# Optimization experiments

Measured on AMD Instinct MI355X. Metric: run time of the kernel, lower is better.

## Reference

```python
import jax, jax.numpy as jnp
import numpy as np

D, H, F, L = 3, 3, 2048, 12  # d_model, nhead, dim_feedforward (torch default), num_layers
EPS = 1e-5


def _ln(x, w, b):
    m = x.mean(-1, keepdims=True)
    v = ((x - m) ** 2).mean(-1, keepdims=True)
    return (x - m) / jnp.sqrt(v + EPS) * w + b


def _mha(q_in, k_in, v_in, w, b, ow, ob):
    # w: [3D, D] packed qkv in_proj (torch layout), x: [T, B, D] seq-first
    qw, kw, vw = w[:D], w[D:2 * D], w[2 * D:]
    qb, kb, vb = b[:D], b[D:2 * D], b[2 * D:]
    q = q_in @ qw.T + qb
    k = k_in @ kw.T + kb
    v = v_in @ vw.T + vb
    hd = D // H  # head_dim = 1
    qh = q.reshape(q.shape[0], q.shape[1], H, hd)
    kh = k.reshape(k.shape[0], k.shape[1], H, hd)
    vh = v.reshape(v.shape[0], v.shape[1], H, hd)
    scores = jnp.einsum('qbhd,kbhd->bhqk', qh, kh) / np.sqrt(hd)
    attn = jax.nn.softmax(scores, axis=-1)
    o = jnp.einsum('bhqk,kbhd->qbhd', attn, vh).reshape(q_in.shape)
    return o @ ow.T + ob


def _encode(x, p):
    # post-norm TransformerEncoderLayer x12, then final encoder LayerNorm
    for i in range(L):
        x = _ln(x + _mha(x, x, x, p['sa_w'][i], p['sa_b'][i], p['sa_ow'][i], p['sa_ob'][i]),
                p['n1_w'][i], p['n1_b'][i])
        h = jax.nn.relu(x @ p['l1_w'][i].T + p['l1_b'][i]) @ p['l2_w'][i].T + p['l2_b'][i]
        x = _ln(x + h, p['n2_w'][i], p['n2_b'][i])
    return _ln(x, p['nf_w'], p['nf_b'])


def _decode(x, mem, p):
    # post-norm TransformerDecoderLayer x12 (no masks, matching the source), final LayerNorm
    for i in range(L):
        x = _ln(x + _mha(x, x, x, p['sa_w'][i], p['sa_b'][i], p['sa_ow'][i], p['sa_ob'][i]),
                p['n1_w'][i], p['n1_b'][i])
        x = _ln(x + _mha(x, mem, mem, p['ca_w'][i], p['ca_b'][i], p['ca_ow'][i], p['ca_ob'][i]),
                p['n2_w'][i], p['n2_b'][i])
        h = jax.nn.relu(x @ p['l1_w'][i].T + p['l1_b'][i]) @ p['l2_w'][i].T + p['l2_b'][i]
        x = _ln(x + h, p['n3_w'][i], p['n3_b'][i])
    return _ln(x, p['nf_w'], p['nf_b'])


def setup_inputs() -> dict:
    key = jax.random.key(0)
    ks = iter(jax.random.split(key, 64))

    def rn(shape, scale=0.1):
        return jax.random.normal(next(ks), shape, jnp.float32) * scale

    B, C, T = 16, 2, 32
    inp = {'src': rn((B, C, T), 1.0), 'angle': rn((B,), 1.0)}
    inp.update(dict(
        enc_sa_w=rn((L, 3 * D, D)), enc_sa_b=rn((L, 3 * D)), enc_sa_ow=rn((L, D, D)), enc_sa_ob=rn((L, D)),
        enc_l1_w=rn((L, F, D)), enc_l1_b=rn((L, F)), enc_l2_w=rn((L, D, F)), enc_l2_b=rn((L, D)),
        enc_n1_w=jnp.ones((L, D)), enc_n1_b=jnp.zeros((L, D)),
        enc_n2_w=jnp.ones((L, D)), enc_n2_b=jnp.zeros((L, D)),
        enc_nf_w=jnp.ones((D,)), enc_nf_b=jnp.zeros((D,)),
        dec_sa_w=rn((L, 3 * D, D)), dec_sa_b=rn((L, 3 * D)), dec_sa_ow=rn((L, D, D)), dec_sa_ob=rn((L, D)),
        dec_ca_w=rn((L, 3 * D, D)), dec_ca_b=rn((L, 3 * D)), dec_ca_ow=rn((L, D, D)), dec_ca_ob=rn((L, D)),
        dec_l1_w=rn((L, F, D)), dec_l1_b=rn((L, F)), dec_l2_w=rn((L, D, F)), dec_l2_b=rn((L, D)),
        dec_n1_w=jnp.ones((L, D)), dec_n1_b=jnp.zeros((L, D)),
        dec_n2_w=jnp.ones((L, D)), dec_n2_b=jnp.zeros((L, D)),
        dec_n3_w=jnp.ones((L, D)), dec_n3_b=jnp.zeros((L, D)),
        dec_nf_w=jnp.ones((D,)), dec_nf_b=jnp.zeros((D,)),
    ))
    return inp


def reference(src, angle,
              enc_sa_w, enc_sa_b, enc_sa_ow, enc_sa_ob, enc_l1_w, enc_l1_b, enc_l2_w, enc_l2_b,
              enc_n1_w, enc_n1_b, enc_n2_w, enc_n2_b, enc_nf_w, enc_nf_b,
              dec_sa_w, dec_sa_b, dec_sa_ow, dec_sa_ob, dec_ca_w, dec_ca_b, dec_ca_ow, dec_ca_ob,
              dec_l1_w, dec_l1_b, dec_l2_w, dec_l2_b,
              dec_n1_w, dec_n1_b, dec_n2_w, dec_n2_b, dec_n3_w, dec_n3_b, dec_nf_w, dec_nf_b):
    enc = dict(sa_w=enc_sa_w, sa_b=enc_sa_b, sa_ow=enc_sa_ow, sa_ob=enc_sa_ob,
               l1_w=enc_l1_w, l1_b=enc_l1_b, l2_w=enc_l2_w, l2_b=enc_l2_b,
               n1_w=enc_n1_w, n1_b=enc_n1_b, n2_w=enc_n2_w, n2_b=enc_n2_b,
               nf_w=enc_nf_w, nf_b=enc_nf_b)
    dec = dict(sa_w=dec_sa_w, sa_b=dec_sa_b, sa_ow=dec_sa_ow, sa_ob=dec_sa_ob,
               ca_w=dec_ca_w, ca_b=dec_ca_b, ca_ow=dec_ca_ow, ca_ob=dec_ca_ob,
               l1_w=dec_l1_w, l1_b=dec_l1_b, l2_w=dec_l2_w, l2_b=dec_l2_b,
               n1_w=dec_n1_w, n1_b=dec_n1_b, n2_w=dec_n2_w, n2_b=dec_n2_b,
               n3_w=dec_n3_w, n3_b=dec_n3_b, nf_w=dec_nf_w, nf_b=dec_nf_b)
    B, _, T = src.shape
    ang = jnp.broadcast_to(angle.reshape(B, 1, 1), (B, 1, T))
    s = jnp.concatenate([src, ang], axis=1)       # [B, 3, T]
    s = jnp.transpose(s, (2, 0, 1))                # [T, B, 3] seq-first
    mem = _encode(s, enc)                          # encoder depends only on src: compute once
    out0 = jnp.zeros_like(s).at[0].set(s[0])

    def step(out, t):
        pred = _decode(out, mem, dec)              # full no-mask decoder, as in the torch loop
        return out.at[t].set(pred[t]), None

    out, _ = jax.lax.scan(step, out0, jnp.arange(1, T))
    return jnp.transpose(out, (1, 2, 0))           # [B, 3, T]
```

## Files before the change

### kernel.cpp

```cpp
#include <hip/hip_runtime.h>
#include <math.h>

#define FF 2048
#define NL 12
#define NB 16
#define TT 32
#define EPS 1e-5f
#define LOG2E 1.44269504088896f

#if __has_builtin(__builtin_amdgcn_exp2f)
#define EXP2(x) __builtin_amdgcn_exp2f(x)
#else
#define EXP2(x) exp2f(x)
#endif

typedef float v2f __attribute__((ext_vector_type(2)));
__device__ __forceinline__ v2f mk2(float x){ v2f r; r.x = x; r.y = x; return r; }

__global__ __launch_bounds__(256) void prepack_kernel(
    const float* __restrict__ enc_l1_w, const float* __restrict__ enc_l1_b,
    const float* __restrict__ enc_l2_w,
    const float* __restrict__ dec_l1_w, const float* __restrict__ dec_l1_b,
    const float* __restrict__ dec_l2_w,
    float4* __restrict__ w_all)
{
    int idx = blockIdx.x * blockDim.x + threadIdx.x;
    if (idx >= 24 * 1024) return;
    int lay = idx >> 10;
    int fp  = idx & 1023;
    int f0  = 2*fp, f1 = 2*fp + 1;
    const float *w1, *b1, *w2;
    if (lay < NL) {
        w1 = enc_l1_w + (size_t)lay * FF * 3;
        b1 = enc_l1_b + (size_t)lay * FF;
        w2 = enc_l2_w + (size_t)lay * 3 * FF;
    } else {
        int l = lay - NL;
        w1 = dec_l1_w + (size_t)l * FF * 3;
        b1 = dec_l1_b + (size_t)l * FF;
        w2 = dec_l2_w + (size_t)l * 3 * FF;
    }
    float4* base = w_all + (size_t)lay * 4096;
    base[fp]        = make_float4(w1[f0*3+0], w1[f1*3+0], w1[f0*3+1], w1[f1*3+1]);
    base[1024 + fp] = make_float4(w1[f0*3+2], w1[f1*3+2], b1[f0],     b1[f1]);
    base[2048 + fp] = make_float4(w2[f0],     w2[f1],     w2[FF+f0],  w2[FF+f1]);
    base[3072 + fp] = make_float4(w2[2*FF+f0], w2[2*FF+f1], 0.f, 0.f);
}

struct __align__(16) SharedMem {
    float4 wbuf[2][4096];
    float4 x4[TT];
    float4 fred[TT][3];
    float4 outst[TT];
    float4 mem4[TT];
    float  kk[3][TT];
    float  vv[3][TT];
    float4 oo[TT];
    float4 oo2[TT];
    float  ck[NL][3][TT];
    float  cv[NL][3][TT];
};

__device__ __forceinline__ void ln3s(float y0, float y1, float y2,
    const float* __restrict__ w, const float* __restrict__ b,
    float& o0, float& o1, float& o2)
{
    float m  = (y0 + y1 + y2) * (1.0f / 3.0f);
    float d0 = y0 - m, d1 = y1 - m, d2 = y2 - m;
    float v  = (d0*d0 + d1*d1 + d2*d2) * (1.0f / 3.0f);
    float r  = __builtin_amdgcn_rsqf(v + EPS);
    o0 = d0 * r * w[0] + b[0];
    o1 = d1 * r * w[1] + b[1];
    o2 = d2 * r * w[2] + b[2];
}

template<int CTRL>
__device__ __forceinline__ float dpp_add(float v)
{
    int sh = __builtin_amdgcn_update_dpp(0, __float_as_int(v), CTRL, 0xF, 0xF, true);
    return v + __int_as_float(sh);
}

__device__ __forceinline__ float wave_sum64(float v)
{
    v = dpp_add<0x111>(v);
    v = dpp_add<0x112>(v);
    v = dpp_add<0x114>(v);
    v = dpp_add<0x118>(v);
    v = dpp_add<0x142>(v);
    v = dpp_add<0x143>(v);
    return v;
}

__device__ __forceinline__ float sum4(float4 r)
{
    return (r.x + r.y) + (r.z + r.w);
}

template<bool MASK>
__device__ __forceinline__ float attn_half(float qs,
    const float* __restrict__ k, const float* __restrict__ v,
    int half, int ntok, int rep, float repw)
{
    const float4* k4 = (const float4*)k;
    const float4* v4 = (const float4*)v;
    float den0 = 0.f, den1 = 0.f, nv0 = 0.f, nv1 = 0.f;
    #pragma unroll
    for (int jb = 0; jb < 4; ++jb) {
        float4 kq = k4[half*4 + jb];
        float4 vq = v4[half*4 + jb];
        const float kj[4] = {kq.x, kq.y, kq.z, kq.w};
        const float vj[4] = {vq.x, vq.y, vq.z, vq.w};
        #pragma unroll
        for (int u = 0; u < 4; ++u) {
            float w = EXP2(qs * kj[u]);
            if (MASK) {
                const int j = half*16 + jb*4 + u;
                w = (j < ntok) ? w : 0.f;
                w = (j == rep) ? w * repw : w;
            }
            if (jb & 1) { den1 += w; nv1 = fmaf(w, vj[u], nv1); }
            else        { den0 += w; nv0 = fmaf(w, vj[u], nv0); }
        }
    }
    float den = den0 + den1;
    float nv  = nv0 + nv1;
    den += __shfl_xor(den, 32, 64);
    nv  += __shfl_xor(nv , 32, 64);
    return nv * __builtin_amdgcn_rcpf(den);
}

template<int NII>
__device__ __forceinline__ void ffn_body(SharedMem& s, int tid,
    const float4* __restrict__ wb)
{
    const int flane = tid & 255;
    const int g     = tid >> 8;
    const int w4    = (tid >> 6) & 3;
    const int lane  = tid & 63;
    const v2f z2 = {0.f, 0.f};
    float X0[NII], X1[NII], X2[NII];
    v2f ac0[NII], ac1[NII], ac2[NII];
    #pragma unroll
    for (int ii = 0; ii < NII; ++ii) {
        float4 xt = s.x4[g + 4*ii];
        X0[ii] = xt.x; X1[ii] = xt.y; X2[ii] = xt.z;
        ac0[ii] = z2; ac1[ii] = z2; ac2[ii] = z2;
    }
    #pragma unroll
    for (int jp = 0; jp < 4; ++jp) {
        const int fp = flane + 256*jp;
        float4 A0 = wb[fp], A1 = wb[1024+fp];
        float4 C0 = wb[2048+fp], C1 = wb[3072+fp];
        v2f ax = {A0.x, A0.y}, ay = {A0.z, A0.w};
        v2f az = {A1.x, A1.y}, ab = {A1.z, A1.w};
        v2f cx = {C0.x, C0.y}, cy = {C0.z, C0.w};
        v2f cz = {C1.x, C1.y};
        #pragma unroll
        for (int ii = 0; ii < NII; ++ii) {
            v2f h2 = __builtin_elementwise_fma(ax, mk2(X0[ii]),
                     __builtin_elementwise_fma(ay, mk2(X1[ii]),
                     __builtin_elementwise_fma(az, mk2(X2[ii]), ab)));
            h2 = __builtin_elementwise_max(h2, z2);
            ac0[ii] = __builtin_elementwise_fma(cx, h2, ac0[ii]);
            ac1[ii] = __builtin_elementwise_fma(cy, h2, ac1[ii]);
            ac2[ii] = __builtin_elementwise_fma(cz, h2, ac2[ii]);
        }
    }
    #pragma unroll
    for (int ii = 0; ii < NII; ++ii) {
        const int t = g + 4*ii;
        float r0 = wave_sum64(ac0[ii].x + ac0[ii].y);
        float r1 = wave_sum64(ac1[ii].x + ac1[ii].y);
        float r2 = wave_sum64(ac2[ii].x + ac2[ii].y);
        if (lane == 63) {
            ((float*)&s.fred[t][0])[w4] = r0;
            ((float*)&s.fred[t][1])[w4] = r1;
            ((float*)&s.fred[t][2])[w4] = r2;
        }
    }
}

template<bool HAS_CA, bool MASK_SA>
__device__ __forceinline__ void run_layer(SharedMem& s, int tid,
    int ntok, int rep, float repw, int do_combine, int p,
    const float4* __restrict__ nw,
    const float* __restrict__ saw, const float* __restrict__ sab,
    const float* __restrict__ saow, const float* __restrict__ saob,
    const float* __restrict__ n1w, const float* __restrict__ n1b,
    const float* __restrict__ caw, const float* __restrict__ cab,
    const float* __restrict__ caow, const float* __restrict__ caob,
    const float* __restrict__ n2w, const float* __restrict__ n2b,
    const float* __restrict__ ckh, const float* __restrict__ cvh,
    const float* __restrict__ pl2b, const float* __restrict__ pnw,
    const float* __restrict__ pnb)
{
    const int wv   = tid >> 6;
    const int lane = tid & 63;
    const int q    = lane & 31;
    const int half = lane >> 5;
    float X0 = 0.f, X1 = 0.f, X2 = 0.f;
    float B0 = 0.f, B1 = 0.f, B2 = 0.f;

    if (wv >= 3) {
        for (int k = tid - 192; k < 2048; k += 832)
            s.wbuf[p ^ 1][k] = nw[k];
    } else {
        const int h = wv;
        float4 xa = s.x4[q];
        if (do_combine) {
            float f0 = sum4(s.fred[q][0]);
            float f1 = sum4(s.fred[q][1]);
            float f2 = sum4(s.fred[q][2]);
            ln3s(xa.x + f0 + pl2b[0], xa.y + f1 + pl2b[1],
                 xa.z + f2 + pl2b[2], pnw, pnb, X0, X1, X2);
        } else { X0 = xa.x; X1 = xa.y; X2 = xa.z; }
        if (lane < 32 && q < ntok) {
            s.kk[h][q] = sab[3+h] + saw[9+3*h]*X0  + saw[10+3*h]*X1 + saw[11+3*h]*X2;
            s.vv[h][q] = sab[6+h] + saw[18+3*h]*X0 + saw[19+3*h]*X1 + saw[20+3*h]*X2;
        }
        float qv = (sab[h] + saw[3*h]*X0 + saw[3*h+1]*X1 + saw[3*h+2]*X2) * LOG2E;
        float o = attn_half<MASK_SA>(qv, s.kk[h], s.vv[h], half, ntok, rep, repw);
        if (lane < 32 && q < ntok) ((float*)&s.oo[q])[h] = o;
    }
    __syncthreads();
    if (wv >= 3) {
        for (int k = 2048 + tid - 192; k < 4096; k += 832)
            s.wbuf[p ^ 1][k] = nw[k];
    } else {
        const int h = wv;
        float4 ov = s.oo[q];
        float y0 = X0 + saob[0] + saow[0]*ov.x + saow[1]*ov.y + saow[2]*ov.z;
        float y1 = X1 + saob[1] + saow[3]*ov.x + saow[4]*ov.y + saow[5]*ov.z;
        float y2 = X2 + saob[2] + saow[6]*ov.x + saow[7]*ov.y + saow[8]*ov.z;
        ln3s(y0, y1, y2, n1w, n1b, B0, B1, B2);
        if (!HAS_CA) {
            if (wv == 0 && lane < 32 && q < ntok)
                s.x4[q] = make_float4(B0, B1, B2, 0.f);
        } else {
            float cqv = (cab[h] + caw[3*h]*B0 + caw[3*h+1]*B1 + caw[3*h+2]*B2) * LOG2E;
            float oc = attn_half<false>(cqv, ckh + h*TT, cvh + h*TT, half, TT, -1, 1.f);
            if (lane < 32 && q < ntok) ((float*)&s.oo2[q])[h] = oc;
        }
    }
    __syncthreads();
    if (HAS_CA) {
        if (wv == 0 && lane < 32 && q < ntok) {
            float4 cv2 = s.oo2[q];
            float y0 = B0 + caob[0] + caow[0]*cv2.x + caow[1]*cv2.y + caow[2]*cv2.z;
            float y1 = B1 + caob[1] + caow[3]*cv2.x + caow[4]*cv2.y + caow[5]*cv2.z;
            float y2 = B2 + caob[2] + caow[6]*cv2.x + caow[7]*cv2.y + caow[8]*cv2.z;
            float a0, a1, a2;
            ln3s(y0, y1, y2, n2w, n2b, a0, a1, a2);
            s.x4[q] = make_float4(a0, a1, a2, 0.f);
        }
        __syncthreads();
    }
    const float4* wb = s.wbuf[p];
    if (ntok <= 8)       ffn_body<2>(s, tid, wb);
    else if (ntok <= 16) ffn_body<4>(s, tid, wb);
    else                 ffn_body<8>(s, tid, wb);
    __syncthreads();
}

__global__ __launch_bounds__(1024, 4) void seq_kernel(
    const float* __restrict__ src, const float* __restrict__ angle,
    const float* __restrict__ enc_sa_w, const float* __restrict__ enc_sa_b,
    const float* __restrict__ enc_sa_ow, const float* __restrict__ enc_sa_ob,
    const float* __restrict__ enc_l2_b,
    const float* __restrict__ enc_n1_w, const float* __restrict__ enc_n1_b,
    const float* __restrict__ enc_n2_w, const float* __restrict__ enc_n2_b,
    const float* __restrict__ enc_nf_w, const float* __restrict__ enc_nf_b,
    const float* __restrict__ dec_sa_w, const float* __restrict__ dec_sa_b,
    const float* __restrict__ dec_sa_ow, const float* __restrict__ dec_sa_ob,
    const float* __restrict__ dec_ca_w, const float* __restrict__ dec_ca_b,
    const float* __restrict__ dec_ca_ow, const float* __restrict__ dec_ca_ob,
    const float* __restrict__ dec_l2_b,
    const float* __restrict__ dec_n1_w, const float* __restrict__ dec_n1_b,
    const float* __restrict__ dec_n2_w, const float* __restrict__ dec_n2_b,
    const float* __restrict__ dec_n3_w, const float* __restrict__ dec_n3_b,
    const float* __restrict__ dec_nf_w, const float* __restrict__ dec_nf_b,
    const float4* __restrict__ w_all,
    float* __restrict__ out)
{
    __shared__ SharedMem s;
    const int tid = threadIdx.x;
    const int b   = blockIdx.x;

    for (int k = tid; k < 4096; k += 1024)
        s.wbuf[0][k] = w_all[k];
    if (tid < TT) {
        float x0 = src[b*64 + tid];
        float x1 = src[b*64 + 32 + tid];
        float x2 = angle[b];
        s.x4[tid] = make_float4(x0, x1, x2, 0.f);
        if (tid == 0) s.outst[0] = make_float4(x0, x1, x2, 0.f);
    }
    __syncthreads();

    int lp = 0;
    for (int i = 0; i < NL; ++i) {
        const float4* nw = w_all + (size_t)((i < 11) ? (i + 1) : 12) * 4096;
        const int pi = (i > 0) ? (i - 1) : 0;
        run_layer<false, false>(s, tid, TT, -1, 1.f, i > 0, lp & 1, nw,
            enc_sa_w + i*27, enc_sa_b + i*9, enc_sa_ow + i*9, enc_sa_ob + i*3,
            enc_n1_w + i*3, enc_n1_b + i*3,
            nullptr, nullptr, nullptr, nullptr, nullptr, nullptr,
            nullptr, nullptr,
            enc_l2_b + pi*3, enc_n2_w + pi*3, enc_n2_b + pi*3);
        ++lp;
    }
    if (tid < 32) {
        float4 xa = s.x4[tid];
        float f0 = sum4(s.fred[tid][0]);
        float f1 = sum4(s.fred[tid][1]);
        float f2 = sum4(s.fred[tid][2]);
        float o0, o1, o2, m0, m1, m2;
        ln3s(xa.x + f0 + enc_l2_b[33], xa.y + f1 + enc_l2_b[34],
             xa.z + f2 + enc_l2_b[35], enc_n2_w + 33, enc_n2_b + 33, o0, o1, o2);
        ln3s(o0, o1, o2, enc_nf_w, enc_nf_b, m0, m1, m2);
        s.mem4[tid] = make_float4(m0, m1, m2, 0.f);
        s.x4[tid]   = (tid == 0) ? s.outst[0] : make_float4(0.f, 0.f, 0.f, 0.f);
    }
    __syncthreads();

    for (int idx = tid; idx < NL * 96; idx += 1024) {
        const int lyr = idx / 96;
        const int r   = idx - lyr * 96;
        const int hh  = r >> 5;
        const int t   = r & 31;
        const float* w  = dec_ca_w + lyr*27;
        const float* bb = dec_ca_b + lyr*9;
        float4 mr = s.mem4[t];
        s.ck[lyr][hh][t] = bb[3+hh] + w[(3+hh)*3]*mr.x + w[(3+hh)*3+1]*mr.y + w[(3+hh)*3+2]*mr.z;
        s.cv[lyr][hh][t] = bb[6+hh] + w[(6+hh)*3]*mr.x + w[(6+hh)*3+1]*mr.y + w[(6+hh)*3+2]*mr.z;
    }
    __syncthreads();

    for (int t = 1; t < TT; ++t) {
        const int ntok = t + 1;
        for (int i = 0; i < NL; ++i) {
            const float4* nw = w_all + (size_t)(12 + ((i < 11) ? (i + 1) : 0)) * 4096;
            const int pi = (i > 0) ? (i - 1) : 0;
            run_layer<true, true>(s, tid, ntok, t, (float)(TT - t), i > 0, lp & 1, nw,
                dec_sa_w + i*27, dec_sa_b + i*9, dec_sa_ow + i*9, dec_sa_ob + i*3,
                dec_n1_w + i*3, dec_n1_b + i*3,
                dec_ca_w + i*27, dec_ca_b + i*9, dec_ca_ow + i*9, dec_ca_ob + i*3,
                dec_n2_w + i*3, dec_n2_b + i*3,
                &s.ck[i][0][0], &s.cv[i][0][0],
                dec_l2_b + pi*3, dec_n3_w + pi*3, dec_n3_b + pi*3);
            ++lp;
        }
        if (tid < 32) {
            if (tid == 0) {
                float4 xa = s.x4[t];
                float f0 = sum4(s.fred[t][0]);
                float f1 = sum4(s.fred[t][1]);
                float f2 = sum4(s.fred[t][2]);
                float o0, o1, o2, p0, p1, p2;
                ln3s(xa.x + f0 + dec_l2_b[33], xa.y + f1 + dec_l2_b[34],
                     xa.z + f2 + dec_l2_b[35], dec_n3_w + 33, dec_n3_b + 33,
                     o0, o1, o2);
                ln3s(o0, o1, o2, dec_nf_w, dec_nf_b, p0, p1, p2);
                s.outst[t] = make_float4(p0, p1, p2, 0.f);
            }
            s.x4[tid] = (tid <= t) ? s.outst[tid] : make_float4(0.f, 0.f, 0.f, 0.f);
        }
        __syncthreads();
    }

    if (tid < TT) {
        float4 o = s.outst[tid];
        out[b*96 +  0 + tid] = o.x;
        out[b*96 + 32 + tid] = o.y;
        out[b*96 + 64 + tid] = o.z;
    }
}

extern "C" void kernel_launch(void* const* d_in, const int* in_sizes, int n_in,
                              void* d_out, int out_size, void* d_ws, size_t ws_size,
                              hipStream_t stream) {
    const float* src      = (const float*)d_in[0];
    const float* angle    = (const float*)d_in[1];
    const float* enc_sa_w = (const float*)d_in[2];
    const float* enc_sa_b = (const float*)d_in[3];
    const float* enc_sa_ow= (const float*)d_in[4];
    const float* enc_sa_ob= (const float*)d_in[5];
    const float* enc_l1_w = (const float*)d_in[6];
    const float* enc_l1_b = (const float*)d_in[7];
    const float* enc_l2_w = (const float*)d_in[8];
    const float* enc_l2_b = (const float*)d_in[9];
    const float* enc_n1_w = (const float*)d_in[10];
    const float* enc_n1_b = (const float*)d_in[11];
    const float* enc_n2_w = (const float*)d_in[12];
    const float* enc_n2_b = (const float*)d_in[13];
    const float* enc_nf_w = (const float*)d_in[14];
    const float* enc_nf_b = (const float*)d_in[15];
    const float* dec_sa_w = (const float*)d_in[16];
    const float* dec_sa_b = (const float*)d_in[17];
    const float* dec_sa_ow= (const float*)d_in[18];
    const float* dec_sa_ob= (const float*)d_in[19];
    const float* dec_ca_w = (const float*)d_in[20];
    const float* dec_ca_b = (const float*)d_in[21];
    const float* dec_ca_ow= (const float*)d_in[22];
    const float* dec_ca_ob= (const float*)d_in[23];
    const float* dec_l1_w = (const float*)d_in[24];
    const float* dec_l1_b = (const float*)d_in[25];
    const float* dec_l2_w = (const float*)d_in[26];
    const float* dec_l2_b = (const float*)d_in[27];
    const float* dec_n1_w = (const float*)d_in[28];
    const float* dec_n1_b = (const float*)d_in[29];
    const float* dec_n2_w = (const float*)d_in[30];
    const float* dec_n2_b = (const float*)d_in[31];
    const float* dec_n3_w = (const float*)d_in[32];
    const float* dec_n3_b = (const float*)d_in[33];
    const float* dec_nf_w = (const float*)d_in[34];
    const float* dec_nf_b = (const float*)d_in[35];

    float4* w_all = (float4*)d_ws;

    prepack_kernel<<<(24 * 1024 + 255) / 256, 256, 0, stream>>>(
        enc_l1_w, enc_l1_b, enc_l2_w,
        dec_l1_w, dec_l1_b, dec_l2_w,
        w_all);

    seq_kernel<<<NB, 1024, 0, stream>>>(
        src, angle,
        enc_sa_w, enc_sa_b, enc_sa_ow, enc_sa_ob, enc_l2_b,
        enc_n1_w, enc_n1_b, enc_n2_w, enc_n2_b, enc_nf_w, enc_nf_b,
        dec_sa_w, dec_sa_b, dec_sa_ow, dec_sa_ob,
        dec_ca_w, dec_ca_b, dec_ca_ow, dec_ca_ob, dec_l2_b,
        dec_n1_w, dec_n1_b, dec_n2_w, dec_n2_b, dec_n3_w, dec_n3_b,
        dec_nf_w, dec_nf_b,
        (const float4*)w_all,
        (float*)d_out);
}
```

Measured before the change: 1.911 ms.

## Run all attention heads in one wave and keep decoder outputs in registers

Attention and layernorm work for all three heads and the cross-attention now run inside wave 0, with one barrier per layer instead of two or three. The other 15 waves prefetch the next layer's FFN weights during that time. The decoder output state moves from shared memory into per-lane registers and is updated lazily inside the first layer of the next step, which drops the per-step sync and copy. Masked key blocks beyond ntok are skipped and wave 0 gets raised priority. The trade-off is more serial work on a single wave per layer.

```diff
diff --git a/kernel.cpp b/kernel.cpp
--- a/kernel.cpp
+++ b/kernel.cpp
@@ -51,12 +51,9 @@
     float4 wbuf[2][4096];
     float4 x4[TT];
     float4 fred[TT][3];
-    float4 outst[TT];
     float4 mem4[TT];
     float  kk[3][TT];
     float  vv[3][TT];
-    float4 oo[TT];
-    float4 oo2[TT];
     float  ck[NL][3][TT];
     float  cv[NL][3][TT];
 };
@@ -107,20 +104,23 @@
     float den0 = 0.f, den1 = 0.f, nv0 = 0.f, nv1 = 0.f;
     #pragma unroll
     for (int jb = 0; jb < 4; ++jb) {
-        float4 kq = k4[half*4 + jb];
-        float4 vq = v4[half*4 + jb];
-        const float kj[4] = {kq.x, kq.y, kq.z, kq.w};
-        const float vj[4] = {vq.x, vq.y, vq.z, vq.w};
-        #pragma unroll
-        for (int u = 0; u < 4; ++u) {
-            float w = EXP2(qs * kj[u]);
-            if (MASK) {
-                const int j = half*16 + jb*4 + u;
-                w = (j < ntok) ? w : 0.f;
-                w = (j == rep) ? w * repw : w;
+        const int jbase = half*16 + jb*4;
+        if (!MASK || jbase < ntok) {
+            float4 kq = k4[half*4 + jb];
+            float4 vq = v4[half*4 + jb];
+            const float kj[4] = {kq.x, kq.y, kq.z, kq.w};
+            const float vj[4] = {vq.x, vq.y, vq.z, vq.w};
+            #pragma unroll
+            for (int u = 0; u < 4; ++u) {
+                float w = EXP2(qs * kj[u]);
+                if (MASK) {
+                    const int j = jbase + u;
+                    w = (j < ntok) ? w : 0.f;
+                    w = (j == rep) ? w * repw : w;
+                }
+                if (jb & 1) { den1 += w; nv1 = fmaf(w, vj[u], nv1); }
+                else        { den0 += w; nv0 = fmaf(w, vj[u], nv0); }
             }
-            if (jb & 1) { den1 += w; nv1 = fmaf(w, vj[u], nv1); }
-            else        { den0 += w; nv0 = fmaf(w, vj[u], nv0); }
         }
     }
     float den = den0 + den1;
@@ -181,9 +181,9 @@
     }
 }
 
-template<bool HAS_CA, bool MASK_SA>
+template<int MODE, bool HAS_CA, bool MASK_SA>
 __device__ __forceinline__ void run_layer(SharedMem& s, int tid,
-    int ntok, int rep, float repw, int do_combine, int p,
+    int ntok, int rep, float repw, int p,
     const float4* __restrict__ nw,
     const float* __restrict__ saw, const float* __restrict__ sab,
     const float* __restrict__ saow, const float* __restrict__ saob,
@@ -193,69 +193,80 @@
     const float* __restrict__ n2w, const float* __restrict__ n2b,
     const float* __restrict__ ckh, const float* __restrict__ cvh,
     const float* __restrict__ pl2b, const float* __restrict__ pnw,
-    const float* __restrict__ pnb)
+    const float* __restrict__ pnb,
+    const float* __restrict__ nfw, const float* __restrict__ nfb,
+    int tprev, int do_update,
+    float E0, float E1, float E2,
+    float& O0, float& O1, float& O2)
 {
     const int wv   = tid >> 6;
     const int lane = tid & 63;
     const int q    = lane & 31;
     const int half = lane >> 5;
-    float X0 = 0.f, X1 = 0.f, X2 = 0.f;
-    float B0 = 0.f, B1 = 0.f, B2 = 0.f;
-
-    if (wv >= 3) {
-        for (int k = tid - 192; k < 2048; k += 832)
+
+    if (wv >= 1) {
+        for (int k = tid - 64; k < 4096; k += 960)
             s.wbuf[p ^ 1][k] = nw[k];
     } else {
-        const int h = wv;
-        float4 xa = s.x4[q];
-        if (do_combine) {
+        __builtin_amdgcn_s_setprio(1);
+        float X0, X1, X2;
+        if (MODE == 0) {
+            X0 = E0; X1 = E1; X2 = E2;
+        } else if (MODE == 1) {
+            float4 xa = s.x4[q];
             float f0 = sum4(s.fred[q][0]);
             float f1 = sum4(s.fred[q][1]);
             float f2 = sum4(s.fred[q][2]);
             ln3s(xa.x + f0 + pl2b[0], xa.y + f1 + pl2b[1],
                  xa.z + f2 + pl2b[2], pnw, pnb, X0, X1, X2);
-        } else { X0 = xa.x; X1 = xa.y; X2 = xa.z; }
-        if (lane < 32 && q < ntok) {
-            s.kk[h][q] = sab[3+h] + saw[9+3*h]*X0  + saw[10+3*h]*X1 + saw[11+3*h]*X2;
-            s.vv[h][q] = sab[6+h] + saw[18+3*h]*X0 + saw[19+3*h]*X1 + saw[20+3*h]*X2;
-        }
-        float qv = (sab[h] + saw[3*h]*X0 + saw[3*h+1]*X1 + saw[3*h+2]*X2) * LOG2E;
-        float o = attn_half<MASK_SA>(qv, s.kk[h], s.vv[h], half, ntok, rep, repw);
-        if (lane < 32 && q < ntok) ((float*)&s.oo[q])[h] = o;
+        } else {
+            if (do_update && q == tprev) {
+                float4 xa = s.x4[q];
+                float f0 = sum4(s.fred[q][0]);
+                float f1 = sum4(s.fred[q][1]);
+                float f2 = sum4(s.fred[q][2]);
+                float o0, o1, o2;
+                ln3s(xa.x + f0 + pl2b[0], xa.y + f1 + pl2b[1],
+                     xa.z + f2 + pl2b[2], pnw, pnb, o0, o1, o2);
+                ln3s(o0, o1, o2, nfw, nfb, O0, O1, O2);
+            }
+            const bool rl = (q <= tprev);
+            X0 = rl ? O0 : 0.f; X1 = rl ? O1 : 0.f; X2 = rl ? O2 : 0.f;
+        }
+        if (half == 0 && q < ntok) {
+            for (int h = 0; h < 3; ++h) {
+                s.kk[h][q] = sab[3+h] + saw[9+3*h]*X0  + saw[10+3*h]*X1 + saw[11+3*h]*X2;
+                s.vv[h][q] = sab[6+h] + saw[18+3*h]*X0 + saw[19+3*h]*X1 + saw[20+3*h]*X2;
+            }
+        }
+        float oh[3];
+        for (int h = 0; h < 3; ++h) {
+            float qv = (sab[h] + saw[3*h]*X0 + saw[3*h+1]*X1 + saw[3*h+2]*X2) * LOG2E;
+            oh[h] = attn_half<MASK_SA>(qv, s.kk[h], s.vv[h], half, ntok, rep, repw);
+        }
+        float y0 = X0 + saob[0] + saow[0]*oh[0] + saow[1]*oh[1] + saow[2]*oh[2];
+        float y1 = X1 + saob[1] + saow[3]*oh[0] + saow[4]*oh[1] + saow[5]*oh[2];
+        float y2 = X2 + saob[2] + saow[6]*oh[0] + saow[7]*oh[1] + saow[8]*oh[2];
+        float B0, B1, B2;
+        ln3s(y0, y1, y2, n1w, n1b, B0, B1, B2);
+        if (HAS_CA) {
+            float oc[3];
+            for (int h = 0; h < 3; ++h) {
+                float cqv = (cab[h] + caw[3*h]*B0 + caw[3*h+1]*B1 + caw[3*h+2]*B2) * LOG2E;
+                oc[h] = attn_half<false>(cqv, ckh + h*TT, cvh + h*TT, half, TT, -1, 1.f);
+            }
+            float z0 = B0 + caob[0] + caow[0]*oc[0] + caow[1]*oc[1] + caow[2]*oc[2];
+            float z1 = B1 + caob[1] + caow[3]*oc[0] + caow[4]*oc[1] + caow[5]*oc[2];
+            float z2 = B2 + caob[2] + caow[6]*oc[0] + caow[7]*oc[1] + caow[8]*oc[2];
+            float A0, A1, A2;
+            ln3s(z0, z1, z2, n2w, n2b, A0, A1, A2);
+            if (half == 0 && q < ntok) s.x4[q] = make_float4(A0, A1, A2, 0.f);
+        } else {
+            if (half == 0 && q < ntok) s.x4[q] = make_float4(B0, B1, B2, 0.f);
+        }
+        __builtin_amdgcn_s_setprio(0);
     }
     __syncthreads();
-    if (wv >= 3) {
-        for (int k = 2048 + tid - 192; k < 4096; k += 832)
-            s.wbuf[p ^ 1][k] = nw[k];
-    } else {
-        const int h = wv;
-        float4 ov = s.oo[q];
-        float y0 = X0 + saob[0] + saow[0]*ov.x + saow[1]*ov.y + saow[2]*ov.z;
-        float y1 = X1 + saob[1] + saow[3]*ov.x + saow[4]*ov.y + saow[5]*ov.z;
-        float y2 = X2 + saob[2] + saow[6]*ov.x + saow[7]*ov.y + saow[8]*ov.z;
-        ln3s(y0, y1, y2, n1w, n1b, B0, B1, B2);
-        if (!HAS_CA) {
-            if (wv == 0 && lane < 32 && q < ntok)
-                s.x4[q] = make_float4(B0, B1, B2, 0.f);
-        } else {
-            float cqv = (cab[h] + caw[3*h]*B0 + caw[3*h+1]*B1 + caw[3*h+2]*B2) * LOG2E;
-            float oc = attn_half<false>(cqv, ckh + h*TT, cvh + h*TT, half, TT, -1, 1.f);
-            if (lane < 32 && q < ntok) ((float*)&s.oo2[q])[h] = oc;
-        }
-    }
-    __syncthreads();
-    if (HAS_CA) {
-        if (wv == 0 && lane < 32 && q < ntok) {
-            float4 cv2 = s.oo2[q];
-            float y0 = B0 + caob[0] + caow[0]*cv2.x + caow[1]*cv2.y + caow[2]*cv2.z;
-            float y1 = B1 + caob[1] + caow[3]*cv2.x + caow[4]*cv2.y + caow[5]*cv2.z;
-            float y2 = B2 + caob[2] + caow[6]*cv2.x + caow[7]*cv2.y + caow[8]*cv2.z;
-            float a0, a1, a2;
-            ln3s(y0, y1, y2, n2w, n2b, a0, a1, a2);
-            s.x4[q] = make_float4(a0, a1, a2, 0.f);
-        }
-        __syncthreads();
-    }
     const float4* wb = s.wbuf[p];
     if (ntok <= 8)       ffn_body<2>(s, tid, wb);
     else if (ntok <= 16) ffn_body<4>(s, tid, wb);
@@ -289,38 +300,54 @@
 
     for (int k = tid; k < 4096; k += 1024)
         s.wbuf[0][k] = w_all[k];
-    if (tid < TT) {
-        float x0 = src[b*64 + tid];
-        float x1 = src[b*64 + 32 + tid];
-        float x2 = angle[b];
-        s.x4[tid] = make_float4(x0, x1, x2, 0.f);
-        if (tid == 0) s.outst[0] = make_float4(x0, x1, x2, 0.f);
-    }
-    __syncthreads();
+
+    float E0 = 0.f, E1 = 0.f, E2 = 0.f, O0 = 0.f, O1 = 0.f, O2 = 0.f;
+    if (tid < 64) {
+        const int q = tid & 31;
+        E0 = src[b*64 + q];
+        E1 = src[b*64 + 32 + q];
+        E2 = angle[b];
+    }
 
     int lp = 0;
-    for (int i = 0; i < NL; ++i) {
+    {
+        const float4* nw0 = w_all + (size_t)1 * 4096;
+        run_layer<0, false, false>(s, tid, TT, -1, 1.f, 0, nw0,
+            enc_sa_w, enc_sa_b, enc_sa_ow, enc_sa_ob,
+            enc_n1_w, enc_n1_b,
+            nullptr, nullptr, nullptr, nullptr, nullptr, nullptr,
+            nullptr, nullptr,
+            nullptr, nullptr, nullptr, nullptr, nullptr,
+            -1, 0, E0, E1, E2, O0, O1, O2);
+        ++lp;
+    }
+    for (int i = 1; i < NL; ++i) {
         const float4* nw = w_all + (size_t)((i < 11) ? (i + 1) : 12) * 4096;
-        const int pi = (i > 0) ? (i - 1) : 0;
-        run_layer<false, false>(s, tid, TT, -1, 1.f, i > 0, lp & 1, nw,
+        run_layer<1, false, false>(s, tid, TT, -1, 1.f, lp & 1, nw,
             enc_sa_w + i*27, enc_sa_b + i*9, enc_sa_ow + i*9, enc_sa_ob + i*3,
             enc_n1_w + i*3, enc_n1_b + i*3,
             nullptr, nullptr, nullptr, nullptr, nullptr, nullptr,
             nullptr, nullptr,
-            enc_l2_b + pi*3, enc_n2_w + pi*3, enc_n2_b + pi*3);
+            enc_l2_b + (i-1)*3, enc_n2_w + (i-1)*3, enc_n2_b + (i-1)*3,
+            nullptr, nullptr,
+            -1, 0, 0.f, 0.f, 0.f, O0, O1, O2);
         ++lp;
     }
-    if (tid < 32) {
-        float4 xa = s.x4[tid];
-        float f0 = sum4(s.fred[tid][0]);
-        float f1 = sum4(s.fred[tid][1]);
-        float f2 = sum4(s.fred[tid][2]);
+
+    if (tid < 64) {
+        const int q = tid & 31;
+        float4 xa = s.x4[q];
+        float f0 = sum4(s.fred[q][0]);
+        float f1 = sum4(s.fred[q][1]);
+        float f2 = sum4(s.fred[q][2]);
         float o0, o1, o2, m0, m1, m2;
         ln3s(xa.x + f0 + enc_l2_b[33], xa.y + f1 + enc_l2_b[34],
              xa.z + f2 + enc_l2_b[35], enc_n2_w + 33, enc_n2_b + 33, o0, o1, o2);
         ln3s(o0, o1, o2, enc_nf_w, enc_nf_b, m0, m1, m2);
-        s.mem4[tid] = make_float4(m0, m1, m2, 0.f);
-        s.x4[tid]   = (tid == 0) ? s.outst[0] : make_float4(0.f, 0.f, 0.f, 0.f);
+        if (tid < 32) s.mem4[q] = make_float4(m0, m1, m2, 0.f);
+        O0 = (q == 0) ? E0 : 0.f;
+        O1 = (q == 0) ? E1 : 0.f;
+        O2 = (q == 0) ? E2 : 0.f;
     }
     __syncthreads();
 
@@ -339,41 +366,53 @@
 
     for (int t = 1; t < TT; ++t) {
         const int ntok = t + 1;
-        for (int i = 0; i < NL; ++i) {
+        const float rw = (float)(TT - t);
+        {
+            const float4* nw = w_all + (size_t)13 * 4096;
+            run_layer<2, true, true>(s, tid, ntok, t, rw, lp & 1, nw,
+                dec_sa_w, dec_sa_b, dec_sa_ow, dec_sa_ob,
+                dec_n1_w, dec_n1_b,
+                dec_ca_w, dec_ca_b, dec_ca_ow, dec_ca_ob,
+                dec_n2_w, dec_n2_b,
+                &s.ck[0][0][0], &s.cv[0][0][0],
+                dec_l2_b + 33, dec_n3_w + 33, dec_n3_b + 33,
+                dec_nf_w, dec_nf_b,
+                t - 1, (t >= 2) ? 1 : 0, 0.f, 0.f, 0.f, O0, O1, O2);
+            ++lp;
+        }
+        for (int i = 1; i < NL; ++i) {
             const float4* nw = w_all + (size_t)(12 + ((i < 11) ? (i + 1) : 0)) * 4096;
-            const int pi = (i > 0) ? (i - 1) : 0;
-            run_layer<true, true>(s, tid, ntok, t, (float)(TT - t), i > 0, lp & 1, nw,
+            run_layer<1, true, true>(s, tid, ntok, t, rw, lp & 1, nw,
                 dec_sa_w + i*27, dec_sa_b + i*9, dec_sa_ow + i*9, dec_sa_ob + i*3,
                 dec_n1_w + i*3, dec_n1_b + i*3,
                 dec_ca_w + i*27, dec_ca_b + i*9, dec_ca_ow + i*9, dec_ca_ob + i*3,
                 dec_n2_w + i*3, dec_n2_b + i*3,
                 &s.ck[i][0][0], &s.cv[i][0][0],
-                dec_l2_b + pi*3, dec_n3_w + pi*3, dec_n3_b + pi*3);
+                dec_l2_b + (i-1)*3, dec_n3_w + (i-1)*3, dec_n3_b + (i-1)*3,
+                nullptr, nullptr,
+                -1, 0, 0.f, 0.f, 0.f, O0, O1, O2);
             ++lp;
         }
+    }
+
+    if (tid < 64) {
+        const int q = tid & 31;
+        if (q == 31) {
+            float4 xa = s.x4[31];
+            float f0 = sum4(s.fred[31][0]);
+            float f1 = sum4(s.fred[31][1]);
+            float f2 = sum4(s.fred[31][2]);
+            float o0, o1, o2;
+            ln3s(xa.x + f0 + dec_l2_b[33], xa.y + f1 + dec_l2_b[34],
+                 xa.z + f2 + dec_l2_b[35], dec_n3_w + 33, dec_n3_b + 33,
+                 o0, o1, o2);
+            ln3s(o0, o1, o2, dec_nf_w, dec_nf_b, O0, O1, O2);
+        }
         if (tid < 32) {
-            if (tid == 0) {
-                float4 xa = s.x4[t];
-                float f0 = sum4(s.fred[t][0]);
-                float f1 = sum4(s.fred[t][1]);
-                float f2 = sum4(s.fred[t][2]);
-                float o0, o1, o2, p0, p1, p2;
-                ln3s(xa.x + f0 + dec_l2_b[33], xa.y + f1 + dec_l2_b[34],
-                     xa.z + f2 + dec_l2_b[35], dec_n3_w + 33, dec_n3_b + 33,
-                     o0, o1, o2);
-                ln3s(o0, o1, o2, dec_nf_w, dec_nf_b, p0, p1, p2);
-                s.outst[t] = make_float4(p0, p1, p2, 0.f);
-            }
-            s.x4[tid] = (tid <= t) ? s.outst[tid] : make_float4(0.f, 0.f, 0.f, 0.f);
-        }
-        __syncthreads();
-    }
-
-    if (tid < TT) {
-        float4 o = s.outst[tid];
-        out[b*96 +  0 + tid] = o.x;
-        out[b*96 + 32 + tid] = o.y;
-        out[b*96 + 64 + tid] = o.z;
+            out[b*96 +  0 + q] = O0;
+            out[b*96 + 32 + q] = O1;
+            out[b*96 + 64 + q] = O2;
+        }
     }
 }
 
```

After: 2.711 ms. 41.9% more time.

## Process two batch elements per block sharing FFN weight buffers

Applied to the files above, without the earlier changes.

Each 1024-thread block now handles two batch elements, so the grid shrinks from 16 to 8 blocks. Waves 0-2 and 3-5 run attention for element 0 and element 1, and the remaining waves prefetch the next layer's FFN weights. The FFN splits threads into two halves, one per element, each streaming all 2048 hidden units from the same shared weight buffer. The goal is to halve global weight traffic and barrier count per element, at the cost of half as many threads working on each element. Attention also skips key blocks past ntok.

```diff
diff --git a/kernel.cpp b/kernel.cpp
--- a/kernel.cpp
+++ b/kernel.cpp
@@ -49,16 +49,16 @@
 
 struct __align__(16) SharedMem {
     float4 wbuf[2][4096];
-    float4 x4[TT];
-    float4 fred[TT][3];
-    float4 outst[TT];
-    float4 mem4[TT];
-    float  kk[3][TT];
-    float  vv[3][TT];
-    float4 oo[TT];
-    float4 oo2[TT];
-    float  ck[NL][3][TT];
-    float  cv[NL][3][TT];
+    float4 x4[2][TT];
+    float  fred[2][TT][3][2];
+    float4 outst[2][TT];
+    float4 mem4[2][TT];
+    float  kk[2][3][TT];
+    float  vv[2][3][TT];
+    float4 oo[2][TT];
+    float4 oo2[2][TT];
+    float  ck[2][NL][3][TT];
+    float  cv[2][NL][3][TT];
 };
 
 __device__ __forceinline__ void ln3s(float y0, float y1, float y2,
@@ -92,10 +92,7 @@
     return v;
 }
 
-__device__ __forceinline__ float sum4(float4 r)
-{
-    return (r.x + r.y) + (r.z + r.w);
-}
+__device__ __forceinline__ float fr2(const float* p) { return p[0] + p[1]; }
 
 template<bool MASK>
 __device__ __forceinline__ float attn_half(float qs,
@@ -107,20 +104,23 @@
     float den0 = 0.f, den1 = 0.f, nv0 = 0.f, nv1 = 0.f;
     #pragma unroll
     for (int jb = 0; jb < 4; ++jb) {
-        float4 kq = k4[half*4 + jb];
-        float4 vq = v4[half*4 + jb];
-        const float kj[4] = {kq.x, kq.y, kq.z, kq.w};
-        const float vj[4] = {vq.x, vq.y, vq.z, vq.w};
-        #pragma unroll
-        for (int u = 0; u < 4; ++u) {
-            float w = EXP2(qs * kj[u]);
-            if (MASK) {
-                const int j = half*16 + jb*4 + u;
-                w = (j < ntok) ? w : 0.f;
-                w = (j == rep) ? w * repw : w;
+        const int jbase = half*16 + jb*4;
+        if (!MASK || jbase < ntok) {
+            float4 kq = k4[half*4 + jb];
+            float4 vq = v4[half*4 + jb];
+            const float kj[4] = {kq.x, kq.y, kq.z, kq.w};
+            const float vj[4] = {vq.x, vq.y, vq.z, vq.w};
+            #pragma unroll
+            for (int u = 0; u < 4; ++u) {
+                float w = EXP2(qs * kj[u]);
+                if (MASK) {
+                    const int j = jbase + u;
+                    w = (j < ntok) ? w : 0.f;
+                    w = (j == rep) ? w * repw : w;
+                }
+                if (jb & 1) { den1 += w; nv1 = fmaf(w, vj[u], nv1); }
+                else        { den0 += w; nv0 = fmaf(w, vj[u], nv0); }
             }
-            if (jb & 1) { den1 += w; nv1 = fmaf(w, vj[u], nv1); }
-            else        { den0 += w; nv0 = fmaf(w, vj[u], nv0); }
         }
     }
     float den = den0 + den1;
@@ -131,25 +131,26 @@
 }
 
 template<int NII>
-__device__ __forceinline__ void ffn_body(SharedMem& s, int tid,
+__device__ __forceinline__ void ffn_body2(SharedMem& s, int tid,
     const float4* __restrict__ wb)
 {
-    const int flane = tid & 255;
-    const int g     = tid >> 8;
-    const int w4    = (tid >> 6) & 3;
+    const int flane = tid & 127;
+    const int gi    = (tid >> 7) & 3;
+    const int e     = tid >> 9;
+    const int w2i   = (tid >> 6) & 1;
     const int lane  = tid & 63;
     const v2f z2 = {0.f, 0.f};
     float X0[NII], X1[NII], X2[NII];
     v2f ac0[NII], ac1[NII], ac2[NII];
     #pragma unroll
     for (int ii = 0; ii < NII; ++ii) {
-        float4 xt = s.x4[g + 4*ii];
+        float4 xt = s.x4[e][gi + 4*ii];
         X0[ii] = xt.x; X1[ii] = xt.y; X2[ii] = xt.z;
         ac0[ii] = z2; ac1[ii] = z2; ac2[ii] = z2;
     }
-    #pragma unroll
-    for (int jp = 0; jp < 4; ++jp) {
-        const int fp = flane + 256*jp;
+    #pragma unroll 2
+    for (int jp = 0; jp < 8; ++jp) {
+        const int fp = flane + 128*jp;
         float4 A0 = wb[fp], A1 = wb[1024+fp];
         float4 C0 = wb[2048+fp], C1 = wb[3072+fp];
         v2f ax = {A0.x, A0.y}, ay = {A0.z, A0.w};
@@ -169,21 +170,21 @@
     }
     #pragma unroll
     for (int ii = 0; ii < NII; ++ii) {
-        const int t = g + 4*ii;
+        const int t = gi + 4*ii;
         float r0 = wave_sum64(ac0[ii].x + ac0[ii].y);
         float r1 = wave_sum64(ac1[ii].x + ac1[ii].y);
         float r2 = wave_sum64(ac2[ii].x + ac2[ii].y);
         if (lane == 63) {
-            ((float*)&s.fred[t][0])[w4] = r0;
-            ((float*)&s.fred[t][1])[w4] = r1;
-            ((float*)&s.fred[t][2])[w4] = r2;
+            s.fred[e][t][0][w2i] = r0;
+            s.fred[e][t][1][w2i] = r1;
+            s.fred[e][t][2][w2i] = r2;
         }
     }
 }
 
 template<bool HAS_CA, bool MASK_SA>
 __device__ __forceinline__ void run_layer(SharedMem& s, int tid,
-    int ntok, int rep, float repw, int do_combine, int p,
+    int ntok, int rep, float repw, int do_combine, int p, int li,
     const float4* __restrict__ nw,
     const float* __restrict__ saw, const float* __restrict__ sab,
     const float* __restrict__ saow, const float* __restrict__ saob,
@@ -191,7 +192,6 @@
     const float* __restrict__ caw, const float* __restrict__ cab,
     const float* __restrict__ caow, const float* __restrict__ caob,
     const float* __restrict__ n2w, const float* __restrict__ n2b,
-    const float* __restrict__ ckh, const float* __restrict__ cvh,
     const float* __restrict__ pl2b, const float* __restrict__ pnw,
     const float* __restrict__ pnb)
 {
@@ -199,67 +199,69 @@
     const int lane = tid & 63;
     const int q    = lane & 31;
     const int half = lane >> 5;
+    const int e    = (wv >= 3) ? 1 : 0;
+    const int h    = wv - 3*e;
     float X0 = 0.f, X1 = 0.f, X2 = 0.f;
     float B0 = 0.f, B1 = 0.f, B2 = 0.f;
 
-    if (wv >= 3) {
-        for (int k = tid - 192; k < 2048; k += 832)
+    if (wv >= 6) {
+        for (int k = tid - 384; k < 2048; k += 640)
             s.wbuf[p ^ 1][k] = nw[k];
     } else {
-        const int h = wv;
-        float4 xa = s.x4[q];
+        float4 xa = s.x4[e][q];
         if (do_combine) {
-            float f0 = sum4(s.fred[q][0]);
-            float f1 = sum4(s.fred[q][1]);
-            float f2 = sum4(s.fred[q][2]);
+            float f0 = fr2(s.fred[e][q][0]);
+            float f1 = fr2(s.fred[e][q][1]);
+            float f2 = fr2(s.fred[e][q][2]);
             ln3s(xa.x + f0 + pl2b[0], xa.y + f1 + pl2b[1],
                  xa.z + f2 + pl2b[2], pnw, pnb, X0, X1, X2);
         } else { X0 = xa.x; X1 = xa.y; X2 = xa.z; }
         if (lane < 32 && q < ntok) {
-            s.kk[h][q] = sab[3+h] + saw[9+3*h]*X0  + saw[10+3*h]*X1 + saw[11+3*h]*X2;
-            s.vv[h][q] = sab[6+h] + saw[18+3*h]*X0 + saw[19+3*h]*X1 + saw[20+3*h]*X2;
+            s.kk[e][h][q] = sab[3+h] + saw[9+3*h]*X0  + saw[10+3*h]*X1 + saw[11+3*h]*X2;
+            s.vv[e][h][q] = sab[6+h] + saw[18+3*h]*X0 + saw[19+3*h]*X1 + saw[20+3*h]*X2;
         }
         float qv = (sab[h] + saw[3*h]*X0 + saw[3*h+1]*X1 + saw[3*h+2]*X2) * LOG2E;
-        float o = attn_half<MASK_SA>(qv, s.kk[h], s.vv[h], half, ntok, rep, repw);
-        if (lane < 32 && q < ntok) ((float*)&s.oo[q])[h] = o;
-    }
-    __syncthreads();
-    if (wv >= 3) {
-        for (int k = 2048 + tid - 192; k < 4096; k += 832)
+        float o = attn_half<MASK_SA>(qv, &s.kk[e][h][0], &s.vv[e][h][0],
+                                     half, ntok, rep, repw);
+        if (lane < 32 && q < ntok) ((float*)&s.oo[e][q])[h] = o;
+    }
+    __syncthreads();
+    if (wv >= 6) {
+        for (int k = 2048 + tid - 384; k < 4096; k += 640)
             s.wbuf[p ^ 1][k] = nw[k];
     } else {
-        const int h = wv;
-        float4 ov = s.oo[q];
+        float4 ov = s.oo[e][q];
         float y0 = X0 + saob[0] + saow[0]*ov.x + saow[1]*ov.y + saow[2]*ov.z;
         float y1 = X1 + saob[1] + saow[3]*ov.x + saow[4]*ov.y + saow[5]*ov.z;
         float y2 = X2 + saob[2] + saow[6]*ov.x + saow[7]*ov.y + saow[8]*ov.z;
         ln3s(y0, y1, y2, n1w, n1b, B0, B1, B2);
         if (!HAS_CA) {
-            if (wv == 0 && lane < 32 && q < ntok)
-                s.x4[q] = make_float4(B0, B1, B2, 0.f);
+            if (h == 0 && lane < 32 && q < ntok)
+                s.x4[e][q] = make_float4(B0, B1, B2, 0.f);
         } else {
             float cqv = (cab[h] + caw[3*h]*B0 + caw[3*h+1]*B1 + caw[3*h+2]*B2) * LOG2E;
-            float oc = attn_half<false>(cqv, ckh + h*TT, cvh + h*TT, half, TT, -1, 1.f);
-            if (lane < 32 && q < ntok) ((float*)&s.oo2[q])[h] = oc;
+            float oc = attn_half<false>(cqv, &s.ck[e][li][h][0], &s.cv[e][li][h][0],
+                                        half, TT, -1, 1.f);
+            if (lane < 32 && q < ntok) ((float*)&s.oo2[e][q])[h] = oc;
         }
     }
     __syncthreads();
     if (HAS_CA) {
-        if (wv == 0 && lane < 32 && q < ntok) {
-            float4 cv2 = s.oo2[q];
+        if (wv < 6 && h == 0 && lane < 32 && q < ntok) {
+            float4 cv2 = s.oo2[e][q];
             float y0 = B0 + caob[0] + caow[0]*cv2.x + caow[1]*cv2.y + caow[2]*cv2.z;
             float y1 = B1 + caob[1] + caow[3]*cv2.x + caow[4]*cv2.y + caow[5]*cv2.z;
             float y2 = B2 + caob[2] + caow[6]*cv2.x + caow[7]*cv2.y + caow[8]*cv2.z;
             float a0, a1, a2;
             ln3s(y0, y1, y2, n2w, n2b, a0, a1, a2);
-            s.x4[q] = make_float4(a0, a1, a2, 0.f);
+            s.x4[e][q] = make_float4(a0, a1, a2, 0.f);
         }
         __syncthreads();
     }
     const float4* wb = s.wbuf[p];
-    if (ntok <= 8)       ffn_body<2>(s, tid, wb);
-    else if (ntok <= 16) ffn_body<4>(s, tid, wb);
-    else                 ffn_body<8>(s, tid, wb);
+    if (ntok <= 8)       ffn_body2<2>(s, tid, wb);
+    else if (ntok <= 16) ffn_body2<4>(s, tid, wb);
+    else                 ffn_body2<8>(s, tid, wb);
     __syncthreads();
 }
 
@@ -285,16 +287,18 @@
 {
     __shared__ SharedMem s;
     const int tid = threadIdx.x;
-    const int b   = blockIdx.x;
+    const int b0  = blockIdx.x * 2;
 
     for (int k = tid; k < 4096; k += 1024)
         s.wbuf[0][k] = w_all[k];
-    if (tid < TT) {
-        float x0 = src[b*64 + tid];
-        float x1 = src[b*64 + 32 + tid];
-        float x2 = angle[b];
-        s.x4[tid] = make_float4(x0, x1, x2, 0.f);
-        if (tid == 0) s.outst[0] = make_float4(x0, x1, x2, 0.f);
+    if (tid < 64) {
+        const int e = tid >> 5;
+        const int q = tid & 31;
+        float x0 = src[(b0 + e)*64 + q];
+        float x1 = src[(b0 + e)*64 + 32 + q];
+        float x2 = angle[b0 + e];
+        s.x4[e][q] = make_float4(x0, x1, x2, 0.f);
+        if (q == 0) s.outst[e][0] = make_float4(x0, x1, x2, 0.f);
     }
     __syncthreads();
 
@@ -302,38 +306,42 @@
     for (int i = 0; i < NL; ++i) {
         const float4* nw = w_all + (size_t)((i < 11) ? (i + 1) : 12) * 4096;
         const int pi = (i > 0) ? (i - 1) : 0;
-        run_layer<false, false>(s, tid, TT, -1, 1.f, i > 0, lp & 1, nw,
+        run_layer<false, false>(s, tid, TT, -1, 1.f, i > 0, lp & 1, 0, nw,
             enc_sa_w + i*27, enc_sa_b + i*9, enc_sa_ow + i*9, enc_sa_ob + i*3,
             enc_n1_w + i*3, enc_n1_b + i*3,
             nullptr, nullptr, nullptr, nullptr, nullptr, nullptr,
-            nullptr, nullptr,
             enc_l2_b + pi*3, enc_n2_w + pi*3, enc_n2_b + pi*3);
         ++lp;
     }
-    if (tid < 32) {
-        float4 xa = s.x4[tid];
-        float f0 = sum4(s.fred[tid][0]);
-        float f1 = sum4(s.fred[tid][1]);
-        float f2 = sum4(s.fred[tid][2]);
+    if (tid < 256 && (tid >> 6) % 3 == 0 && (tid & 63) < 32) {
+        const int wv = tid >> 6;
+        const int e  = wv / 3;
+        const int q  = tid & 31;
+        float4 xa = s.x4[e][q];
+        float f0 = fr2(s.fred[e][q][0]);
+        float f1 = fr2(s.fred[e][q][1]);
+        float f2 = fr2(s.fred[e][q][2]);
         float o0, o1, o2, m0, m1, m2;
         ln3s(xa.x + f0 + enc_l2_b[33], xa.y + f1 + enc_l2_b[34],
              xa.z + f2 + enc_l2_b[35], enc_n2_w + 33, enc_n2_b + 33, o0, o1, o2);
         ln3s(o0, o1, o2, enc_nf_w, enc_nf_b, m0, m1, m2);
-        s.mem4[tid] = make_float4(m0, m1, m2, 0.f);
-        s.x4[tid]   = (tid == 0) ? s.outst[0] : make_float4(0.f, 0.f, 0.f, 0.f);
-    }
-    __syncthreads();
-
-    for (int idx = tid; idx < NL * 96; idx += 1024) {
-        const int lyr = idx / 96;
-        const int r   = idx - lyr * 96;
+        s.mem4[e][q] = make_float4(m0, m1, m2, 0.f);
+        s.x4[e][q]   = (q == 0) ? s.outst[e][0] : make_float4(0.f, 0.f, 0.f, 0.f);
+    }
+    __syncthreads();
+
+    for (int idx = tid; idx < 2 * NL * 96; idx += 1024) {
+        const int e   = idx / (NL * 96);
+        const int r0  = idx - e * NL * 96;
+        const int lyr = r0 / 96;
+        const int r   = r0 - lyr * 96;
         const int hh  = r >> 5;
         const int t   = r & 31;
         const float* w  = dec_ca_w + lyr*27;
         const float* bb = dec_ca_b + lyr*9;
-        float4 mr = s.mem4[t];
-        s.ck[lyr][hh][t] = bb[3+hh] + w[(3+hh)*3]*mr.x + w[(3+hh)*3+1]*mr.y + w[(3+hh)*3+2]*mr.z;
-        s.cv[lyr][hh][t] = bb[6+hh] + w[(6+hh)*3]*mr.x + w[(6+hh)*3+1]*mr.y + w[(6+hh)*3+2]*mr.z;
+        float4 mr = s.mem4[e][t];
+        s.ck[e][lyr][hh][t] = bb[3+hh] + w[(3+hh)*3]*mr.x + w[(3+hh)*3+1]*mr.y + w[(3+hh)*3+2]*mr.z;
+        s.cv[e][lyr][hh][t] = bb[6+hh] + w[(6+hh)*3]*mr.x + w[(6+hh)*3+1]*mr.y + w[(6+hh)*3+2]*mr.z;
     }
     __syncthreads();
 
@@ -342,38 +350,45 @@
         for (int i = 0; i < NL; ++i) {
             const float4* nw = w_all + (size_t)(12 + ((i < 11) ? (i + 1) : 0)) * 4096;
             const int pi = (i > 0) ? (i - 1) : 0;
-            run_layer<true, true>(s, tid, ntok, t, (float)(TT - t), i > 0, lp & 1, nw,
+            run_layer<true, true>(s, tid, ntok, t, (float)(TT - t), i > 0, lp & 1, i, nw,
                 dec_sa_w + i*27, dec_sa_b + i*9, dec_sa_ow + i*9, dec_sa_ob + i*3,
                 dec_n1_w + i*3, dec_n1_b + i*3,
                 dec_ca_w + i*27, dec_ca_b + i*9, dec_ca_ow + i*9, dec_ca_ob + i*3,
                 dec_n2_w + i*3, dec_n2_b + i*3,
-                &s.ck[i][0][0], &s.cv[i][0][0],
                 dec_l2_b + pi*3, dec_n3_w + pi*3, dec_n3_b + pi*3);
             ++lp;
         }
-        if (tid < 32) {
-            if (tid == 0) {
-                float4 xa = s.x4[t];
-                float f0 = sum4(s.fred[t][0]);
-                float f1 = sum4(s.fred[t][1]);
-                float f2 = sum4(s.fred[t][2]);
-                float o0, o1, o2, p0, p1, p2;
-                ln3s(xa.x + f0 + dec_l2_b[33], xa.y + f1 + dec_l2_b[34],
-                     xa.z + f2 + dec_l2_b[35], dec_n3_w + 33, dec_n3_b + 33,
-                     o0, o1, o2);
-                ln3s(o0, o1, o2, dec_nf_w, dec_nf_b, p0, p1, p2);
-                s.outst[t] = make_float4(p0, p1, p2, 0.f);
+        {
+            const int wv = tid >> 6;
+            if ((wv == 0 || wv == 3) && (tid & 63) < 32) {
+                const int e    = wv / 3;
+                const int lane = tid & 63;
+                if (lane == 0) {
+                    float4 xa = s.x4[e][t];
+                    float f0 = fr2(s.fred[e][t][0]);
+                    float f1 = fr2(s.fred[e][t][1]);
+                    float f2 = fr2(s.fred[e][t][2]);
+                    float o0, o1, o2, p0, p1, p2;
+                    ln3s(xa.x + f0 + dec_l2_b[33], xa.y + f1 + dec_l2_b[34],
+                         xa.z + f2 + dec_l2_b[35], dec_n3_w + 33, dec_n3_b + 33,
+                         o0, o1, o2);
+                    ln3s(o0, o1, o2, dec_nf_w, dec_nf_b, p0, p1, p2);
+                    s.outst[e][t] = make_float4(p0, p1, p2, 0.f);
+                }
+                s.x4[e][lane] = (lane <= t) ? s.outst[e][lane]
+                                            : make_float4(0.f, 0.f, 0.f, 0.f);
             }
-            s.x4[tid] = (tid <= t) ? s.outst[tid] : make_float4(0.f, 0.f, 0.f, 0.f);
         }
         __syncthreads();
     }
 
-    if (tid < TT) {
-        float4 o = s.outst[tid];
-        out[b*96 +  0 + tid] = o.x;
-        out[b*96 + 32 + tid] = o.y;
-        out[b*96 + 64 + tid] = o.z;
+    if (tid < 64) {
+        const int e = tid >> 5;
+        const int q = tid & 31;
+        float4 o = s.outst[e][q];
+        out[(b0 + e)*96 +  0 + q] = o.x;
+        out[(b0 + e)*96 + 32 + q] = o.y;
+        out[(b0 + e)*96 + 64 + q] = o.z;
     }
 }
 
@@ -424,7 +439,7 @@
         dec_l1_w, dec_l1_b, dec_l2_w,
         w_all);
 
-    seq_kernel<<<NB, 1024, 0, stream>>>(
+    seq_kernel<<<NB/2, 1024, 0, stream>>>(
         src, angle,
         enc_sa_w, enc_sa_b, enc_sa_ow, enc_sa_ob, enc_l2_b,
         enc_n1_w, enc_n1_b, enc_n2_w, enc_n2_b, enc_nf_w, enc_nf_b,
```

Result: slower. 2.875 ms (+50.5%).
